# Kernel optimization log

Measured on AMD Instinct MI355X. Metric: run time of the kernel, lower is better.

The kernel has to match this reference:

```python
import jax, jax.numpy as jnp
import numpy as np

B, C, H, T, K = 8, 512, 512, 4096, 2


def _conv1d_causal(x, w, b):
    # x: [B, C, T], w: [H, C, K] (torch Conv1d layout OIH), causal left-pad K-1 zeros
    k = w.shape[-1]
    y = jax.lax.conv_general_dilated(
        x, w, window_strides=(1,), padding=[(k - 1, 0)],
        dimension_numbers=("NCH", "OIH", "NCH"))
    return y + b[None, :, None]


def setup_inputs() -> dict:
    key = jax.random.key(0)
    ks = jax.random.split(key, 5)
    scale = 1.0 / np.sqrt(C * K)  # torch Conv1d default init scale
    inp = {"x": jax.random.normal(ks[0], (B, C, T), dtype=jnp.float32)}
    for name, k in zip("zfoi", ks[1:]):
        inp["w" + name] = jax.random.uniform(k, (H, C, K), jnp.float32, -scale, scale)
        inp["b" + name] = jnp.zeros((H,), jnp.float32)
    return inp


def reference(x, wz, bz, wf, bf, wo, bo, wi, bi):
    # QRNN 'ifo' pooling: c_t = f_t * c_{t-1} + i_t * z_t;  h_t = o_t * c_t
    z = jnp.tanh(_conv1d_causal(x, wz, bz))
    f = jax.nn.sigmoid(_conv1d_causal(x, wf, bf))  # zoneout p=0 -> identity
    o = jax.nn.sigmoid(_conv1d_causal(x, wo, bo))
    i = jax.nn.sigmoid(_conv1d_causal(x, wi, bi))
    g = i * z  # [B, H, T]

    fT = jnp.moveaxis(f, 2, 0)  # [T, B, H]
    gT = jnp.moveaxis(g, 2, 0)

    def step(c, fg):
        ft, gt = fg
        c = ft * c + gt
        return c, c

    c0 = jnp.zeros((x.shape[0], wz.shape[0]), dtype=x.dtype)
    _, cT = jax.lax.scan(step, c0, (fT, gT))
    c = jnp.moveaxis(cT, 0, 2)  # [B, H, T]
    return o * c
```

## Files before the change

kernel.cpp:

```cpp
#include <hip/hip_runtime.h>
#include <hip/hip_bf16.h>
#include <cstdint>

typedef _Float16 half8 __attribute__((ext_vector_type(8)));
typedef float f32x4 __attribute__((ext_vector_type(4)));

#define B_DIM 8
#define C_DIM 512
#define H_DIM 512
#define T_DIM 4096
#define KTOT 1024
#define MTOT 2048

__device__ __forceinline__ void gload16(const void* g, void* l) {
  __builtin_amdgcn_global_load_lds(
      (const __attribute__((address_space(1))) unsigned int*)g,
      (__attribute__((address_space(3))) unsigned int*)l, 16, 0, 0);
}

__device__ __forceinline__ float sigmoidf_(float x) { return 1.0f / (1.0f + expf(-x)); }

__global__ __launch_bounds__(256) void pack_w(
    const float* __restrict__ wz, const float* __restrict__ wf,
    const float* __restrict__ wo, const float* __restrict__ wi,
    _Float16* __restrict__ A16) {
  int idx = blockIdx.x * 256 + threadIdx.x;
  int m = idx >> 10, k = idx & 1023;
  int h = m >> 2, g = m & 3;
  int j = k >> 9, c = k & 511;
  const float* w = (g == 0) ? wz : (g == 1) ? wf : (g == 2) ? wo : wi;
  A16[idx] = (_Float16)w[(h << 10) + (c << 1) + j];
}

__global__ __launch_bounds__(256) void transpose_x(
    const float* __restrict__ x, _Float16* __restrict__ XT) {
  int bid = blockIdx.x;
  int b = bid >> 9;
  int rem = bid & 511;
  int c0 = (rem >> 6) * 64;
  int t0 = (rem & 63) * 64;
  __shared__ _Float16 tile[64][72];
  int tid = threadIdx.x;
#pragma unroll
  for (int it = 0; it < 4; ++it) {
    int idx = it * 256 + tid;
    int ci = idx >> 4, tc = idx & 15;
    float4 v = *(const float4*)(x + (((size_t)b * C_DIM + c0 + ci) * T_DIM + t0 + tc * 4));
    tile[ci][tc * 4 + 0] = (_Float16)v.x;
    tile[ci][tc * 4 + 1] = (_Float16)v.y;
    tile[ci][tc * 4 + 2] = (_Float16)v.z;
    tile[ci][tc * 4 + 3] = (_Float16)v.w;
  }
  __syncthreads();
#pragma unroll
  for (int it = 0; it < 2; ++it) {
    int idx = it * 256 + tid;
    int tr = idx >> 3, cb = idx & 7;
    half8 h;
#pragma unroll
    for (int e = 0; e < 8; ++e) h[e] = tile[cb * 8 + e][tr];
    int t = t0 + tr;
    size_t rowbase = ((size_t)b * T_DIM + t) * KTOT;
    *(half8*)(XT + rowbase + 512 + c0 + cb * 8) = h;
    if (t + 1 < T_DIM)
      *(half8*)(XT + rowbase + KTOT + c0 + cb * 8) = h;
  }
  if (t0 == 0 && tid < 8) {
    half8 z = {};
    *(half8*)(XT + ((size_t)b * T_DIM) * KTOT + c0 + tid * 8) = z;
  }
}

__global__ __launch_bounds__(256, 2) void qrnn_gemm(
    const _Float16* __restrict__ A16, const _Float16* __restrict__ XT,
    const float* __restrict__ bz, const float* __restrict__ bf,
    const float* __restrict__ bo, const float* __restrict__ bi,
    _Float16* __restrict__ F, _Float16* __restrict__ G, _Float16* __restrict__ O) {
  __shared__ _Float16 lA[128 * 64];
  __shared__ _Float16 lB[128 * 64];
  int bid = blockIdx.x;
  int b = bid >> 9;
  int rem = bid & 511;
  int m0 = (rem >> 5) * 128;
  int t0 = (rem & 31) * 128;
  int tid = threadIdx.x;
  int lane = tid & 63, wid = tid >> 6;
  int wm = (wid >> 1) * 64, wn = (wid & 1) * 64;

  f32x4 acc[4][4];
#pragma unroll
  for (int i = 0; i < 4; ++i)
#pragma unroll
    for (int j = 0; j < 4; ++j) acc[i][j] = (f32x4){0.f, 0.f, 0.f, 0.f};

  const _Float16* Ab = A16 + (size_t)m0 * KTOT;
  const _Float16* Bb = XT + ((size_t)b * T_DIM + t0) * KTOT;

  for (int kt = 0; kt < 16; ++kt) {
    int k0 = kt * 64;
#pragma unroll
    for (int it = 0; it < 4; ++it) {
      int idx = it * 256 + tid;
      int row = idx >> 3, blk = idx & 7;
      int gblk = blk ^ (row & 7);
      gload16(Ab + (size_t)row * KTOT + k0 + gblk * 8, (char*)lA + idx * 16);
    }
#pragma unroll
    for (int it = 0; it < 4; ++it) {
      int idx = it * 256 + tid;
      int row = idx >> 3, blk = idx & 7;
      int gblk = blk ^ (row & 7);
      gload16(Bb + (size_t)row * KTOT + k0 + gblk * 8, (char*)lB + idx * 16);
    }
    __syncthreads();
#pragma unroll
    for (int ks = 0; ks < 2; ++ks) {
      half8 av[4], bv[4];
#pragma unroll
      for (int i = 0; i < 4; ++i) {
        int row = wm + i * 16 + (lane & 15);
        int blk = (ks * 4 + (lane >> 4)) ^ (row & 7);
        av[i] = *(const half8*)(lA + row * 64 + blk * 8);
      }
#pragma unroll
      for (int j = 0; j < 4; ++j) {
        int row = wn + j * 16 + (lane & 15);
        int blk = (ks * 4 + (lane >> 4)) ^ (row & 7);
        bv[j] = *(const half8*)(lB + row * 64 + blk * 8);
      }
#pragma unroll
      for (int i = 0; i < 4; ++i)
#pragma unroll
        for (int j = 0; j < 4; ++j)
          acc[i][j] = __builtin_amdgcn_mfma_f32_16x16x32_f16(av[i], bv[j], acc[i][j], 0, 0, 0);
    }
    __syncthreads();
  }

#pragma unroll
  for (int i = 0; i < 4; ++i) {
    int h = ((m0 + wm + i * 16) >> 2) + (lane >> 4);
    float vbz = bz[h], vbf = bf[h], vbo = bo[h], vbi = bi[h];
#pragma unroll
    for (int j = 0; j < 4; ++j) {
      int t = t0 + wn + j * 16 + (lane & 15);
      float yz = acc[i][j][0] + vbz;
      float yf = acc[i][j][1] + vbf;
      float yo = acc[i][j][2] + vbo;
      float yi = acc[i][j][3] + vbi;
      float zz = tanhf(yz);
      float ff = sigmoidf_(yf);
      float oo = sigmoidf_(yo);
      float ii = sigmoidf_(yi);
      size_t gi = ((size_t)b * H_DIM + h) * T_DIM + t;
      F[gi] = (_Float16)ff;
      G[gi] = (_Float16)(ii * zz);
      O[gi] = (_Float16)oo;
    }
  }
}

__global__ __launch_bounds__(256) void scan_chunks(
    const _Float16* __restrict__ F, const _Float16* __restrict__ G,
    float* __restrict__ cF, float* __restrict__ cG) {
  int idx = blockIdx.x * 256 + threadIdx.x;
  int ch = idx & 31;
  size_t bh = idx >> 5;
  const half8* f8 = (const half8*)(F + bh * T_DIM + ch * 128);
  const half8* g8 = (const half8*)(G + bh * T_DIM + ch * 128);
  float Fp = 1.f, Gc = 0.f;
#pragma unroll 4
  for (int t8 = 0; t8 < 16; ++t8) {
    half8 fv = f8[t8], gv = g8[t8];
#pragma unroll
    for (int e = 0; e < 8; ++e) {
      float fe = (float)fv[e];
      Gc = fe * Gc + (float)gv[e];
      Fp *= fe;
    }
  }
  cF[idx] = Fp;
  cG[idx] = Gc;
}

__global__ __launch_bounds__(256) void scan_carry(
    const float* __restrict__ cF, const float* __restrict__ cG, float* __restrict__ cC) {
  int bh = blockIdx.x * 256 + threadIdx.x;
  float c = 0.f;
#pragma unroll
  for (int j = 0; j < 32; ++j) {
    int id = bh * 32 + j;
    cC[id] = c;
    c = cF[id] * c + cG[id];
  }
}

__global__ __launch_bounds__(256) void scan_apply(
    const _Float16* __restrict__ F, const _Float16* __restrict__ G,
    const _Float16* __restrict__ O, const float* __restrict__ cC,
    float* __restrict__ out) {
  int idx = blockIdx.x * 256 + threadIdx.x;
  int ch = idx & 31;
  size_t bh = idx >> 5;
  size_t base = bh * T_DIM + ch * 128;
  const half8* f8 = (const half8*)(F + base);
  const half8* g8 = (const half8*)(G + base);
  const half8* o8 = (const half8*)(O + base);
  float c = cC[idx];
  float4* out4 = (float4*)(out + base);
#pragma unroll 4
  for (int t8 = 0; t8 < 16; ++t8) {
    half8 fv = f8[t8], gv = g8[t8], ov = o8[t8];
    float r[8];
#pragma unroll
    for (int e = 0; e < 8; ++e) {
      c = (float)fv[e] * c + (float)gv[e];
      r[e] = (float)ov[e] * c;
    }
    out4[t8 * 2 + 0] = make_float4(r[0], r[1], r[2], r[3]);
    out4[t8 * 2 + 1] = make_float4(r[4], r[5], r[6], r[7]);
  }
}

extern "C" void kernel_launch(void* const* d_in, const int* in_sizes, int n_in,
                              void* d_out, int out_size, void* d_ws, size_t ws_size,
                              hipStream_t stream) {
  (void)in_sizes; (void)n_in; (void)out_size; (void)ws_size;
  const float* x  = (const float*)d_in[0];
  const float* wz = (const float*)d_in[1];
  const float* bz = (const float*)d_in[2];
  const float* wf = (const float*)d_in[3];
  const float* bf = (const float*)d_in[4];
  const float* wo = (const float*)d_in[5];
  const float* bo = (const float*)d_in[6];
  const float* wi = (const float*)d_in[7];
  const float* bi = (const float*)d_in[8];

  char* ws = (char*)d_ws;
  const size_t MB = 1ull << 20;
  _Float16* A16 = (_Float16*)(ws);
  _Float16* XT  = (_Float16*)(ws + 4 * MB);
  _Float16* F   = (_Float16*)(ws + 68 * MB);
  _Float16* G   = (_Float16*)(ws + 100 * MB);
  _Float16* O   = (_Float16*)(ws + 132 * MB);
  float* cF = (float*)(ws + 164 * MB);
  float* cG = cF + 4096 * 32;
  float* cC = cG + 4096 * 32;

  pack_w<<<(MTOT * KTOT) / 256, 256, 0, stream>>>(wz, wf, wo, wi, A16);
  transpose_x<<<B_DIM * 8 * 64, 256, 0, stream>>>(x, XT);
  qrnn_gemm<<<B_DIM * 16 * 32, 256, 0, stream>>>(A16, XT, bz, bf, bo, bi, F, G, O);
  scan_chunks<<<(4096 * 32) / 256, 256, 0, stream>>>(F, G, cF, cG);
  scan_carry<<<4096 / 256, 256, 0, stream>>>(cF, cG, cC);
  scan_apply<<<(4096 * 32) / 256, 256, 0, stream>>>(F, G, O, cC, (float*)d_out);
}
```

Baseline: 382.5 us.

## Fuse three-pass chunked scan into single per-row block scan with LDS staging

Replaces the chunk-reduce, carry and apply scan kernels with one kernel where each block owns a full (b,h) row of 4096 steps. The block stages F/G/O into LDS with async loads, runs a per-thread serial scan plus a wave shuffle and cross-wave combine, then writes output through a swizzled LDS buffer for coalesced stores. This cuts two launches and the second read of F and G from global memory, at the cost of more LDS use per block. It also pads the transpose tile row from 72 to 73 halves to change LDS bank mapping.

```diff
diff --git a/kernel.cpp b/kernel.cpp
--- a/kernel.cpp
+++ b/kernel.cpp
@@ -39,7 +39,7 @@
   int rem = bid & 511;
   int c0 = (rem >> 6) * 64;
   int t0 = (rem & 63) * 64;
-  __shared__ _Float16 tile[64][72];
+  __shared__ _Float16 tile[64][73];
   int tid = threadIdx.x;
 #pragma unroll
   for (int it = 0; it < 4; ++it) {
@@ -160,65 +160,106 @@
   }
 }
 
-__global__ __launch_bounds__(256) void scan_chunks(
+__global__ __launch_bounds__(256) void scan_fused(
     const _Float16* __restrict__ F, const _Float16* __restrict__ G,
-    float* __restrict__ cF, float* __restrict__ cG) {
-  int idx = blockIdx.x * 256 + threadIdx.x;
-  int ch = idx & 31;
-  size_t bh = idx >> 5;
-  const half8* f8 = (const half8*)(F + bh * T_DIM + ch * 128);
-  const half8* g8 = (const half8*)(G + bh * T_DIM + ch * 128);
+    const _Float16* __restrict__ O, float* __restrict__ out) {
+  __shared__ char smem[24 * 1024 + 64];
+  _Float16* sF = (_Float16*)smem;
+  _Float16* sG = (_Float16*)(smem + 8192);
+  _Float16* sO = (_Float16*)(smem + 16384);
+  float* sOut = (float*)smem;
+  float* wFs = (float*)(smem + 24576);
+  float* wGs = wFs + 4;
+
+  int tid = threadIdx.x;
+  int lane = tid & 63, wv = tid >> 6;
+  size_t base = (size_t)blockIdx.x * T_DIM;
+  const _Float16* Fg = F + base;
+  const _Float16* Gg = G + base;
+  const _Float16* Og = O + base;
+
+#pragma unroll
+  for (int it = 0; it < 2; ++it) {
+    int idx = it * 256 + tid;
+    int sb = idx ^ ((idx >> 3) & 7);
+    gload16(Fg + sb * 8, (char*)sF + idx * 16);
+    gload16(Gg + sb * 8, (char*)sG + idx * 16);
+    gload16(Og + sb * 8, (char*)sO + idx * 16);
+  }
+  asm volatile("s_waitcnt vmcnt(0)");
+  __syncthreads();
+
+  int i = tid;
+  int b0 = (2 * i) ^ (((2 * i) >> 3) & 7);
+  int b1 = (2 * i + 1) ^ (((2 * i + 1) >> 3) & 7);
+  half8 f0 = *(half8*)((char*)sF + b0 * 16);
+  half8 f1 = *(half8*)((char*)sF + b1 * 16);
+  half8 g0 = *(half8*)((char*)sG + b0 * 16);
+  half8 g1 = *(half8*)((char*)sG + b1 * 16);
+  half8 o0 = *(half8*)((char*)sO + b0 * 16);
+  half8 o1 = *(half8*)((char*)sO + b1 * 16);
+
   float Fp = 1.f, Gc = 0.f;
-#pragma unroll 4
-  for (int t8 = 0; t8 < 16; ++t8) {
-    half8 fv = f8[t8], gv = g8[t8];
-#pragma unroll
-    for (int e = 0; e < 8; ++e) {
-      float fe = (float)fv[e];
-      Gc = fe * Gc + (float)gv[e];
-      Fp *= fe;
-    }
-  }
-  cF[idx] = Fp;
-  cG[idx] = Gc;
-}
-
-__global__ __launch_bounds__(256) void scan_carry(
-    const float* __restrict__ cF, const float* __restrict__ cG, float* __restrict__ cC) {
-  int bh = blockIdx.x * 256 + threadIdx.x;
-  float c = 0.f;
-#pragma unroll
-  for (int j = 0; j < 32; ++j) {
-    int id = bh * 32 + j;
-    cC[id] = c;
-    c = cF[id] * c + cG[id];
-  }
-}
-
-__global__ __launch_bounds__(256) void scan_apply(
-    const _Float16* __restrict__ F, const _Float16* __restrict__ G,
-    const _Float16* __restrict__ O, const float* __restrict__ cC,
-    float* __restrict__ out) {
-  int idx = blockIdx.x * 256 + threadIdx.x;
-  int ch = idx & 31;
-  size_t bh = idx >> 5;
-  size_t base = bh * T_DIM + ch * 128;
-  const half8* f8 = (const half8*)(F + base);
-  const half8* g8 = (const half8*)(G + base);
-  const half8* o8 = (const half8*)(O + base);
-  float c = cC[idx];
-  float4* out4 = (float4*)(out + base);
-#pragma unroll 4
-  for (int t8 = 0; t8 < 16; ++t8) {
-    half8 fv = f8[t8], gv = g8[t8], ov = o8[t8];
-    float r[8];
-#pragma unroll
-    for (int e = 0; e < 8; ++e) {
-      c = (float)fv[e] * c + (float)gv[e];
-      r[e] = (float)ov[e] * c;
-    }
-    out4[t8 * 2 + 0] = make_float4(r[0], r[1], r[2], r[3]);
-    out4[t8 * 2 + 1] = make_float4(r[4], r[5], r[6], r[7]);
+#pragma unroll
+  for (int e = 0; e < 8; ++e) {
+    float fe = (float)f0[e];
+    Gc = fe * Gc + (float)g0[e];
+    Fp *= fe;
+  }
+#pragma unroll
+  for (int e = 0; e < 8; ++e) {
+    float fe = (float)f1[e];
+    Gc = fe * Gc + (float)g1[e];
+    Fp *= fe;
+  }
+
+  float Fs = Fp, Gs = Gc;
+#pragma unroll
+  for (int d = 1; d < 64; d <<= 1) {
+    float Fo = __shfl_up(Fs, d);
+    float Go = __shfl_up(Gs, d);
+    if (lane >= d) { Gs = Fs * Go + Gs; Fs = Fs * Fo; }
+  }
+  if (lane == 63) { wFs[wv] = Fs; wGs[wv] = Gs; }
+  __syncthreads();
+  float carry = 0.f;
+  for (int w = 0; w < wv; ++w) carry = wFs[w] * carry + wGs[w];
+  float Fpr = __shfl_up(Fs, 1);
+  float Gpr = __shfl_up(Gs, 1);
+  float cin = (lane == 0) ? carry : Fpr * carry + Gpr;
+
+  float c = cin;
+  float4 r0, r1, r2, r3;
+#define QSTEP(fv, gv, ov, e, dst) \
+  { c = (float)fv[e] * c + (float)gv[e]; dst = (float)ov[e] * c; }
+  QSTEP(f0, g0, o0, 0, r0.x) QSTEP(f0, g0, o0, 1, r0.y)
+  QSTEP(f0, g0, o0, 2, r0.z) QSTEP(f0, g0, o0, 3, r0.w)
+  QSTEP(f0, g0, o0, 4, r1.x) QSTEP(f0, g0, o0, 5, r1.y)
+  QSTEP(f0, g0, o0, 6, r1.z) QSTEP(f0, g0, o0, 7, r1.w)
+  QSTEP(f1, g1, o1, 0, r2.x) QSTEP(f1, g1, o1, 1, r2.y)
+  QSTEP(f1, g1, o1, 2, r2.z) QSTEP(f1, g1, o1, 3, r2.w)
+  QSTEP(f1, g1, o1, 4, r3.x) QSTEP(f1, g1, o1, 5, r3.y)
+  QSTEP(f1, g1, o1, 6, r3.z) QSTEP(f1, g1, o1, 7, r3.w)
+#undef QSTEP
+  {
+    int obl = 4 * i;
+    int s0 = (obl + 0) ^ (((obl + 0) >> 3) & 7);
+    int s1 = (obl + 1) ^ (((obl + 1) >> 3) & 7);
+    int s2 = (obl + 2) ^ (((obl + 2) >> 3) & 7);
+    int s3 = (obl + 3) ^ (((obl + 3) >> 3) & 7);
+    *(float4*)((char*)sOut + s0 * 16) = r0;
+    *(float4*)((char*)sOut + s1 * 16) = r1;
+    *(float4*)((char*)sOut + s2 * 16) = r2;
+    *(float4*)((char*)sOut + s3 * 16) = r3;
+  }
+  __syncthreads();
+
+  float* og = out + base;
+#pragma unroll
+  for (int it = 0; it < 4; ++it) {
+    int idx = it * 256 + tid;
+    int sb = idx ^ ((idx >> 3) & 7);
+    *(float4*)(og + idx * 4) = *(float4*)((char*)sOut + sb * 16);
   }
 }
 
@@ -243,14 +284,9 @@
   _Float16* F   = (_Float16*)(ws + 68 * MB);
   _Float16* G   = (_Float16*)(ws + 100 * MB);
   _Float16* O   = (_Float16*)(ws + 132 * MB);
-  float* cF = (float*)(ws + 164 * MB);
-  float* cG = cF + 4096 * 32;
-  float* cC = cG + 4096 * 32;
 
   pack_w<<<(MTOT * KTOT) / 256, 256, 0, stream>>>(wz, wf, wo, wi, A16);
   transpose_x<<<B_DIM * 8 * 64, 256, 0, stream>>>(x, XT);
   qrnn_gemm<<<B_DIM * 16 * 32, 256, 0, stream>>>(A16, XT, bz, bf, bo, bi, F, G, O);
-  scan_chunks<<<(4096 * 32) / 256, 256, 0, stream>>>(F, G, cF, cG);
-  scan_carry<<<4096 / 256, 256, 0, stream>>>(cF, cG, cC);
-  scan_apply<<<(4096 * 32) / 256, 256, 0, stream>>>(F, G, O, cC, (float*)d_out);
-}
+  scan_fused<<<B_DIM * H_DIM, 256, 0, stream>>>(F, G, O, (float*)d_out);
+}
```

New measurement: 320.3 us. -16.3%, faster.
